# Kernel optimization log

Hardware: AMD Instinct MI355X
Metric: run time of the kernel (lower is better)

Reference implementation:

```python
import jax, jax.numpy as jnp
import numpy as np

H = 4096      # hidden_size
NH = 32       # num heads
HD = H // NH  # head_dim = 128
I = 11008     # intermediate_size
T = 1024      # prompt tokens
G = 128       # AWQ group size
EPS = 1e-6
ROPE_BASE = 10000.0


def _pack4(key, in_f, out_f):
    # pack 8 uint4 nibbles per int32, [in_f, out_f/8]
    nib = jax.random.randint(key, (in_f, out_f // 8, 8), 0, 16, dtype=jnp.int32)
    shifts = (jnp.arange(8, dtype=jnp.int32) * 4)
    return jnp.bitwise_or.reduce(nib << shifts, axis=-1).astype(jnp.int32)


def _dequant(qw, qz, sc):
    # qw:[in,out/8] int32, qz:[in/G,out/8] int32, sc:[in/G,out] float
    shifts = jnp.arange(8, dtype=jnp.int32) * 4
    w = ((qw[:, :, None] >> shifts) & 0xF).reshape(qw.shape[0], -1)   # [in,out]
    z = ((qz[:, :, None] >> shifts) & 0xF).reshape(qz.shape[0], -1)   # [groups,out]
    gidx = jnp.arange(qw.shape[0]) // G
    return (w.astype(sc.dtype) - z.astype(sc.dtype)[gidx]) * sc[gidx]


def _qlinear(x, qw, qz, sc):
    return x @ _dequant(qw, qz, sc)


def _rmsnorm(x, w):
    var = jnp.mean(x * x, axis=-1, keepdims=True)
    return x * jax.lax.rsqrt(var + EPS) * w


def _rope(x, positions):
    # x: [T, NH, HD], neox-style half rotation (vLLM rotary)
    inv = 1.0 / (ROPE_BASE ** (jnp.arange(0, HD, 2, dtype=jnp.float32) / HD))
    freqs = positions.astype(jnp.float32)[:, None] * inv[None, :]     # [T, HD/2]
    cos = jnp.cos(freqs)[:, None, :]
    sin = jnp.sin(freqs)[:, None, :]
    x1, x2 = jnp.split(x, 2, axis=-1)
    return jnp.concatenate([x1 * cos - x2 * sin, x2 * cos + x1 * sin], axis=-1)


def _attention(positions, q, k, v):
    # causal self-attention over the prompt (prefill writes k/v to cache then attends)
    q = _rope(q.reshape(T, NH, HD), positions)
    k = _rope(k.reshape(T, NH, HD), positions)
    v = v.reshape(T, NH, HD)
    scale = HD ** -0.5
    scores = jnp.einsum('qhd,khd->hqk', q, k) * scale
    mask = jnp.tril(jnp.ones((T, T), dtype=bool))
    scores = jnp.where(mask[None], scores, jnp.finfo(scores.dtype).min)
    probs = jax.nn.softmax(scores, axis=-1)
    out = jnp.einsum('hqk,khd->qhd', probs, v)
    return out.reshape(T, NH * HD)


def setup_inputs() -> dict:
    key = jax.random.key(0)
    ks = jax.random.split(key, 16)
    S = 0.002  # AWQ scale magnitude
    inp = {
        'positions': jnp.arange(T, dtype=jnp.int32),
        'hidden_states': jax.random.normal(ks[0], (T, H), dtype=jnp.float32),
        'ln1_w': jnp.ones((H,), dtype=jnp.float32),
        'ln2_w': jnp.ones((H,), dtype=jnp.float32),
        'qkv_qw': _pack4(ks[1], H, 3 * H),
        'qkv_qz': _pack4(ks[2], H // G, 3 * H),
        'qkv_sc': jax.random.uniform(ks[3], (H // G, 3 * H), dtype=jnp.float32) * S,
        'o_qw': _pack4(ks[4], H, H),
        'o_qz': _pack4(ks[5], H // G, H),
        'o_sc': jax.random.uniform(ks[6], (H // G, H), dtype=jnp.float32) * S,
        'gate_qw': _pack4(ks[7], H, I),
        'gate_qz': _pack4(ks[8], H // G, I),
        'gate_sc': jax.random.uniform(ks[9], (H // G, I), dtype=jnp.float32) * S,
        'up_qw': _pack4(ks[10], H, I),
        'up_qz': _pack4(ks[11], H // G, I),
        'up_sc': jax.random.uniform(ks[12], (H // G, I), dtype=jnp.float32) * S,
        'down_qw': _pack4(ks[13], I, H),
        'down_qz': _pack4(ks[14], I // G, H),
        'down_sc': jax.random.uniform(ks[15], (I // G, H), dtype=jnp.float32) * S,
    }
    return inp


def reference(positions, hidden_states, ln1_w, qkv_qw, qkv_qz, qkv_sc,
              o_qw, o_qz, o_sc, gate_qw, gate_qz, gate_sc,
              up_qw, up_qz, up_sc, down_qw, down_qz, down_sc, ln2_w):
    # --- self attention block ---
    residual = hidden_states
    x = _rmsnorm(hidden_states, ln1_w)
    qkv = _qlinear(x, qkv_qw, qkv_qz, qkv_sc)                # [T, 3H]
    q, k, v = jnp.split(qkv, 3, axis=-1)
    attn_out = _attention(positions, q, k, v)                # [T, H]
    x = _qlinear(attn_out, o_qw, o_qz, o_sc)
    hidden = residual + x
    # --- MLP block ---
    residual = hidden
    x = _rmsnorm(hidden, ln2_w)
    gate = jax.nn.silu(_qlinear(x, gate_qw, gate_qz, gate_sc))
    up = _qlinear(x, up_qw, up_qz, up_sc)
    x = _qlinear(gate * up, down_qw, down_qz, down_sc)
    return residual + x
```

## Files before the change

### kernel.cpp

```cpp
#include <hip/hip_runtime.h>
#include <cstdint>

typedef __attribute__((ext_vector_type(8))) short  bf16x8;
typedef __attribute__((ext_vector_type(4))) float  f32x4;
typedef __attribute__((ext_vector_type(4))) unsigned int uint4v;
typedef __attribute__((ext_vector_type(2))) unsigned int uint2v;

typedef const __attribute__((address_space(1))) void* gas_t;
typedef __attribute__((address_space(3))) void* las_t;

__device__ __forceinline__ float bf2f(unsigned short b) {
    union { unsigned int u; float f; } v; v.u = ((unsigned int)b) << 16; return v.f;
}
__device__ __forceinline__ unsigned short f2bf(float f) {
    union { float f; unsigned int u; } v; v.f = f;
    unsigned int r = v.u + 0x7FFFu + ((v.u >> 16) & 1u);
    return (unsigned short)(r >> 16);
}
__device__ __forceinline__ float u2f(unsigned int u) {
    union { unsigned int u; float f; } v; v.u = u; return v.f;
}

__device__ __forceinline__ void dequant_block(int bx, int by, int t,
    const int* __restrict__ qw, const int* __restrict__ qz,
    const float* __restrict__ sc, unsigned short* __restrict__ out,
    int NW, int K)
{
    const int wcb = bx << 5;
    const int kb  = by << 6;
    const int g   = by >> 1;
    const int N   = NW << 3;
    const int wc  = wcb + (t >> 3);
    const int k0  = kb + ((t & 7) << 3);

    unsigned int w[8];
#pragma unroll
    for (int j = 0; j < 8; j++) w[j] = (unsigned int)qw[(size_t)(k0 + j) * NW + wc];
    const unsigned int zw = (unsigned int)qz[(size_t)g * NW + wc];
    float scv[8];
#pragma unroll
    for (int j2 = 0; j2 < 8; j2++) scv[j2] = sc[(size_t)g * N + (wc << 3) + j2];

#pragma unroll
    for (int j2 = 0; j2 < 8; j2++) {
        const int sh = j2 << 2;
        const float s = scv[j2];
        const float moff = -(8388608.0f + (float)((zw >> sh) & 0xFu)) * s;
        unsigned int pk[4];
#pragma unroll
        for (int i = 0; i < 4; i++) {
            float f0 = fmaf(u2f(((w[2*i]   >> sh) & 0xFu) | 0x4B000000u), s, moff);
            float f1 = fmaf(u2f(((w[2*i+1] >> sh) & 0xFu) | 0x4B000000u), s, moff);
            asm("v_cvt_pk_bf16_f32 %0, %1, %2" : "=v"(pk[i]) : "v"(f0), "v"(f1));
        }
        uint4v ov = {pk[0], pk[1], pk[2], pk[3]};
        *(uint4v*)(out + (size_t)((wc << 3) + j2) * K + k0) = ov;
    }
}

__global__ __launch_bounds__(256)
void deq_rms_kernel(const int* __restrict__ qw, const int* __restrict__ qz,
                    const float* __restrict__ sc, unsigned short* __restrict__ wout,
                    int NW, int K, int deqBlocks,
                    const float* __restrict__ x, const float* __restrict__ lnw,
                    unsigned short* __restrict__ xout)
{
    __shared__ float red[4];
    const int tid = threadIdx.x;
    if (blockIdx.x < (unsigned)deqBlocks) {
        int xb = NW >> 5;
        dequant_block(blockIdx.x % xb, blockIdx.x / xb, tid, qw, qz, sc, wout, NW, K);
        return;
    }
    const int t = blockIdx.x - deqBlocks;
    const float4* xr = (const float4*)(x + (size_t)t * 4096);
    float4 v[4];
    float ss = 0.f;
#pragma unroll
    for (int j = 0; j < 4; j++) {
        v[j] = xr[(j << 8) + tid];
        ss += v[j].x*v[j].x + v[j].y*v[j].y + v[j].z*v[j].z + v[j].w*v[j].w;
    }
#pragma unroll
    for (int m = 1; m < 64; m <<= 1) ss += __shfl_xor(ss, m);
    if ((tid & 63) == 0) red[tid >> 6] = ss;
    __syncthreads();
    float tot = red[0] + red[1] + red[2] + red[3];
    float rs = rsqrtf(tot * (1.f / 4096.f) + 1e-6f);
    const float4* wr = (const float4*)lnw;
#pragma unroll
    for (int j = 0; j < 4; j++) {
        float4 wv = wr[(j << 8) + tid];
        float4 xv = v[j];
        unsigned int p0 = (unsigned int)f2bf(xv.x*rs*wv.x) | ((unsigned int)f2bf(xv.y*rs*wv.y) << 16);
        unsigned int p1 = (unsigned int)f2bf(xv.z*rs*wv.z) | ((unsigned int)f2bf(xv.w*rs*wv.w) << 16);
        uint2v pk = {p0, p1};
        *(uint2v*)(&xout[(size_t)t*4096 + (size_t)(((j << 8) + tid) << 2)]) = pk;
    }
}

__global__ __launch_bounds__(256)
void rmsnorm_kernel(const float* __restrict__ x, const float* __restrict__ wgt,
                    unsigned short* __restrict__ out)
{
    const int t = blockIdx.x, tid = threadIdx.x;
    const float4* xr = (const float4*)(x + (size_t)t * 4096);
    float4 v[4];
    float ss = 0.f;
#pragma unroll
    for (int j = 0; j < 4; j++) {
        v[j] = xr[(j << 8) + tid];
        ss += v[j].x*v[j].x + v[j].y*v[j].y + v[j].z*v[j].z + v[j].w*v[j].w;
    }
#pragma unroll
    for (int m = 1; m < 64; m <<= 1) ss += __shfl_xor(ss, m);
    __shared__ float red[4];
    if ((tid & 63) == 0) red[tid >> 6] = ss;
    __syncthreads();
    float tot = red[0] + red[1] + red[2] + red[3];
    float rs = rsqrtf(tot * (1.f / 4096.f) + 1e-6f);
    const float4* wr = (const float4*)wgt;
#pragma unroll
    for (int j = 0; j < 4; j++) {
        float4 wv = wr[(j << 8) + tid];
        float4 xv = v[j];
        unsigned int p0 = (unsigned int)f2bf(xv.x*rs*wv.x) | ((unsigned int)f2bf(xv.y*rs*wv.y) << 16);
        unsigned int p1 = (unsigned int)f2bf(xv.z*rs*wv.z) | ((unsigned int)f2bf(xv.w*rs*wv.w) << 16);
        uint2v pk = {p0, p1};
        *(uint2v*)(&out[(size_t)t*4096 + (size_t)(((j << 8) + tid) << 2)]) = pk;
    }
}

template<int MODE>
__global__ __launch_bounds__(256, 4)
void bt_gemm(const unsigned short* __restrict__ A,
             const unsigned short* __restrict__ Bt0,
             const unsigned short* __restrict__ Bt1,
             void* __restrict__ out0, void* __restrict__ out1,
             const float* __restrict__ res,
             int N, int K, int NB, int gemmBlocks, int ksplit,
             const int* dq1_qw, const int* dq1_qz, const float* dq1_sc,
             unsigned short* dq1_out, int dq1_NW, int dq1_K)
{
    const int flat = blockIdx.x;
    if (flat >= gemmBlocks) {
        if (blockIdx.z != 0) return;
        int db = flat - gemmBlocks;
        int xb = dq1_NW >> 5;
        dequant_block(db % xb, db / xb, threadIdx.x, dq1_qw, dq1_qz, dq1_sc, dq1_out, dq1_NW, dq1_K);
        return;
    }

    const int work = NB * (flat & 7) + (flat >> 3);
    const int n0 = (work >> 3) << 7;
    const int m0 = (work & 7) << 7;
    const int z  = blockIdx.z;

    const unsigned short* Bt = Bt0;
    void* outp = out0;
    if (MODE == 1 && z == 1) { Bt = Bt1; outp = out1; }
    const int k0base = (MODE == 2) ? z * ksplit : 0;
    const int nsteps = ((MODE == 2) ? ksplit : K) >> 6;

    __shared__ unsigned short As[128 * 64];
    __shared__ unsigned short Bs[128 * 64];

    const int tid  = threadIdx.x;
    const int lane = tid & 63;
    const int wid  = tid >> 6;
    const int wm   = wid >> 1, wn = wid & 1;

    f32x4 acc[4][4];
#pragma unroll
    for (int i = 0; i < 4; i++)
#pragma unroll
        for (int j = 0; j < 4; j++) { f32x4 zv = {0.f,0.f,0.f,0.f}; acc[i][j] = zv; }

    for (int t = 0; t < nsteps; t++) {
        const int k0 = k0base + (t << 6);
        __syncthreads();
#pragma unroll
        for (int i = 0; i < 4; i++) {
            int slot = (i << 8) + tid;
            int row = slot >> 3, s = slot & 7;
            __builtin_amdgcn_global_load_lds(
                (gas_t)(A + (size_t)(m0 + row) * K + k0 + ((s ^ (row & 7)) << 3)),
                (las_t)&As[slot << 3], 16, 0, 0);
        }
#pragma unroll
        for (int i = 0; i < 4; i++) {
            int slot = (i << 8) + tid;
            int row = slot >> 3, s = slot & 7;
            __builtin_amdgcn_global_load_lds(
                (gas_t)(Bt + (size_t)(n0 + row) * K + k0 + ((s ^ (row & 7)) << 3)),
                (las_t)&Bs[slot << 3], 16, 0, 0);
        }
        __syncthreads();
#pragma unroll
        for (int kk = 0; kk < 2; kk++) {
            const int srow = (kk << 2) + (lane >> 4);
            bf16x8 af[4], bfv[4];
#pragma unroll
            for (int mi = 0; mi < 4; mi++) {
                int r = (wm << 6) + (mi << 4) + (lane & 15);
                af[mi] = *(const bf16x8*)(&As[(r << 6) + ((srow ^ (r & 7)) << 3)]);
            }
#pragma unroll
            for (int ni = 0; ni < 4; ni++) {
                int r = (wn << 6) + (ni << 4) + (lane & 15);
                bfv[ni] = *(const bf16x8*)(&Bs[(r << 6) + ((srow ^ (r & 7)) << 3)]);
            }
#pragma unroll
            for (int mi = 0; mi < 4; mi++)
#pragma unroll
                for (int ni = 0; ni < 4; ni++)
                    acc[mi][ni] = __builtin_amdgcn_mfma_f32_16x16x32_bf16(af[mi], bfv[ni], acc[mi][ni], 0, 0, 0);
        }
    }

    const int rbase = m0 + (wm << 6) + ((lane >> 4) << 2);
    const int cbase = n0 + (wn << 6) + (lane & 15);
#pragma unroll
    for (int mi = 0; mi < 4; mi++) {
#pragma unroll
        for (int r = 0; r < 4; r++) {
            int row = rbase + (mi << 4) + r;
#pragma unroll
            for (int ni = 0; ni < 4; ni++) {
                int col = cbase + (ni << 4);
                float v = acc[mi][ni][r];
                if (MODE == 3) {
                    ((float*)out0)[(size_t)row * N + col] = v + res[(size_t)row * N + col];
                } else if (MODE == 2) {
                    ((unsigned short*)out0)[(size_t)z * ((size_t)1024 * N) + (size_t)row * N + col] = f2bf(v);
                } else {
                    ((unsigned short*)outp)[(size_t)row * N + col] = f2bf(v);
                }
            }
        }
    }
}

__global__ __launch_bounds__(256)
void reduce4_kernel(const float* __restrict__ base, const unsigned short* __restrict__ part,
                    float* __restrict__ out)
{
    const size_t i = (size_t)blockIdx.x * 256 + threadIdx.x;
    const size_t stride = (size_t)1024 * 4096;
    float s[8];
    float4 a0 = ((const float4*)base)[2*i], a1 = ((const float4*)base)[2*i+1];
    s[0]=a0.x; s[1]=a0.y; s[2]=a0.z; s[3]=a0.w; s[4]=a1.x; s[5]=a1.y; s[6]=a1.z; s[7]=a1.w;
#pragma unroll
    for (int p = 0; p < 4; p++) {
        uint4v v = *(const uint4v*)(part + p * stride + i * 8);
#pragma unroll
        for (int j = 0; j < 4; j++) {
            s[2*j]   += bf2f((unsigned short)(v[j] & 0xFFFF));
            s[2*j+1] += bf2f((unsigned short)(v[j] >> 16));
        }
    }
    float4 o0 = {s[0],s[1],s[2],s[3]}, o1 = {s[4],s[5],s[6],s[7]};
    ((float4*)out)[2*i] = o0; ((float4*)out)[2*i+1] = o1;
}

__global__ __launch_bounds__(256)
void rope_kernel(const int* __restrict__ positions, const unsigned short* __restrict__ qkv,
                 unsigned short* __restrict__ Qr, unsigned short* __restrict__ Kr,
                 unsigned short* __restrict__ Vtp)
{
    const int t = blockIdx.x, tid = threadIdx.x;
    const float p = (float)positions[t];
    const unsigned short* row = qkv + (size_t)t * 12288;
#pragma unroll 4
    for (int it = 0; it < 16; it++) {
        int task = (it << 8) + tid;
        int i   = task & 63;
        int hh  = (task >> 6) & 31;
        int isK = task >> 11;
        float fr = p * __expf(-(float)i * 0.14391156831f);
        float s, c;
        __sincosf(fr, &s, &c);
        const unsigned short* src = row + (isK << 12) + (hh << 7);
        float x1 = bf2f(src[i]);
        float x2 = bf2f(src[64 + i]);
        float o1 = x1 * c - x2 * s;
        float o2 = x2 * c + x1 * s;
        if (!isK) { o1 *= 0.08838834764831845f; o2 *= 0.08838834764831845f; }
        unsigned short* dst = (isK ? Kr : Qr) + ((size_t)hh * 1024 + t) * 128;
        dst[i]      = f2bf(o1);
        dst[64 + i] = f2bf(o2);
    }
#pragma unroll 4
    for (int it = 0; it < 16; it++) {
        int task = (it << 8) + tid;
        int d = task & 127, hh = task >> 7;
        Vtp[((size_t)hh * 128 + d) * 1024 + t] = row[8192 + task];
    }
}

__global__ __launch_bounds__(256, 2)
void attn_kernel(const unsigned short* __restrict__ Qr, const unsigned short* __restrict__ Kr,
                 const unsigned short* __restrict__ Vtp, unsigned short* __restrict__ attn_out,
                 int attnBlocks,
                 const int* __restrict__ dqw, const int* __restrict__ dqz,
                 const float* __restrict__ dsc, unsigned short* __restrict__ dwout,
                 int dNW, int dK)
{
    if (blockIdx.x >= (unsigned)attnBlocks) {
        int db = blockIdx.x - attnBlocks;
        int xb = dNW >> 5;
        dequant_block(db % xb, db / xb, threadIdx.x, dqw, dqz, dsc, dwout, dNW, dK);
        return;
    }
    __shared__ unsigned short Ks[64 * 128];
    __shared__ unsigned short Vs[128 * 64];
    __shared__ unsigned short Ps[4][16 * 64];
    const int tid = threadIdx.x, lane = tid & 63, w = tid >> 6;
    const int qt = blockIdx.x & 15, h = blockIdx.x >> 4;

    const unsigned short* Qh = Qr + ((size_t)h * 1024 + (size_t)qt * 64) * 128;

    bf16x8 qf[4];
#pragma unroll
    for (int kk = 0; kk < 4; kk++)
        qf[kk] = *(const bf16x8*)(Qh + (size_t)((w << 4) + (lane & 15)) * 128 + (kk << 5) + ((lane >> 4) << 3));

    f32x4 o[8];
#pragma unroll
    for (int i = 0; i < 8; i++) { f32x4 zf = {0.f,0.f,0.f,0.f}; o[i] = zf; }
    float Mr[4] = {-1e30f, -1e30f, -1e30f, -1e30f};
    float Lr[4] = {0.f, 0.f, 0.f, 0.f};
    const int qrow0 = (qt << 6) + (w << 4) + ((lane >> 4) << 2);

    for (int kt = 0; kt <= qt; kt++) {
        __syncthreads();
#pragma unroll
        for (int j = 0; j < 4; j++) {
            int slot = (j << 8) + tid;
            int rw = slot >> 4, s = slot & 15;
            int ssrc = (s & 8) | ((s ^ (rw & 7)) & 7);
            const uint4v* src = (const uint4v*)(Kr + ((size_t)h * 1024 + (size_t)kt * 64 + rw) * 128 + (ssrc << 3));
            *(uint4v*)(&Ks[(rw << 7) + (s << 3)]) = *src;
        }
#pragma unroll
        for (int j = 0; j < 4; j++) {
            int slot = (j << 8) + tid;
            int rw = slot >> 3, s = slot & 7;
            const uint4v* src = (const uint4v*)(Vtp + ((size_t)h * 128 + rw) * 1024 + (kt << 6) + ((s ^ (rw & 7)) << 3));
            *(uint4v*)(&Vs[(rw << 6) + (s << 3)]) = *src;
        }
        __syncthreads();

        f32x4 sc4[4];
#pragma unroll
        for (int ni = 0; ni < 4; ni++) { f32x4 zf = {0.f,0.f,0.f,0.f}; sc4[ni] = zf; }
#pragma unroll
        for (int kk = 0; kk < 4; kk++) {
#pragma unroll
            for (int ni = 0; ni < 4; ni++) {
                int r = (ni << 4) + (lane & 15);
                int s = (kk << 2) + (lane >> 4);
                int sp = (s & 8) | ((s ^ (r & 7)) & 7);
                bf16x8 kf = *(const bf16x8*)(&Ks[(r << 7) + (sp << 3)]);
                sc4[ni] = __builtin_amdgcn_mfma_f32_16x16x32_bf16(qf[kk], kf, sc4[ni], 0, 0, 0);
            }
        }

#pragma unroll
        for (int r = 0; r < 4; r++) {
            int qg = qrow0 + r;
            float mx = -1e30f;
#pragma unroll
            for (int ni = 0; ni < 4; ni++) {
                int kg_ = (kt << 6) + (ni << 4) + (lane & 15);
                float v = sc4[ni][r];
                if (kt == qt && kg_ > qg) { v = -1e30f; sc4[ni][r] = v; }
                mx = fmaxf(mx, v);
            }
#pragma unroll
            for (int m_ = 1; m_ < 16; m_ <<= 1) mx = fmaxf(mx, __shfl_xor(mx, m_));
            float mnew  = fmaxf(Mr[r], mx);
            float alpha = __expf(Mr[r] - mnew);
            Mr[r] = mnew;
            float rs = 0.f;
#pragma unroll
            for (int ni = 0; ni < 4; ni++) {
                float pv = __expf(sc4[ni][r] - mnew);
                sc4[ni][r] = pv;
                rs += pv;
            }
#pragma unroll
            for (int m_ = 1; m_ < 16; m_ <<= 1) rs += __shfl_xor(rs, m_);
            Lr[r] = Lr[r] * alpha + rs;
#pragma unroll
            for (int nd = 0; nd < 8; nd++) o[nd][r] *= alpha;
        }

#pragma unroll
        for (int r = 0; r < 4; r++) {
            int qr = ((lane >> 4) << 2) + r;
#pragma unroll
            for (int ni = 0; ni < 4; ni++) {
                int col = (ni << 4) + (lane & 15);
                int phys = (col >> 3) ^ (qr & 7);
                Ps[w][(qr << 6) + (phys << 3) + (col & 7)] = f2bf(sc4[ni][r]);
            }
        }
#pragma unroll
        for (int kk2 = 0; kk2 < 2; kk2++) {
            int rowp = lane & 15;
            int sl = (kk2 << 2) + (lane >> 4);
            bf16x8 pa = *(const bf16x8*)(&Ps[w][(rowp << 6) + ((sl ^ (rowp & 7)) << 3)]);
#pragma unroll
            for (int nd = 0; nd < 8; nd++) {
                int rv = (nd << 4) + (lane & 15);
                bf16x8 vb = *(const bf16x8*)(&Vs[(rv << 6) + ((sl ^ (rv & 7)) << 3)]);
                o[nd] = __builtin_amdgcn_mfma_f32_16x16x32_bf16(pa, vb, o[nd], 0, 0, 0);
            }
        }
    }

#pragma unroll
    for (int r = 0; r < 4; r++) {
        float inv = 1.0f / Lr[r];
        int trow = qrow0 + r;
#pragma unroll
        for (int nd = 0; nd < 8; nd++) {
            int col = (h << 7) + (nd << 4) + (lane & 15);
            attn_out[(size_t)trow * 4096 + col] = f2bf(o[nd][r] * inv);
        }
    }
}

__global__ __launch_bounds__(256)
void silu_deq_kernel(const unsigned short* __restrict__ gate, unsigned short* __restrict__ up,
                     int siluBlocks,
                     const int* __restrict__ qw, const int* __restrict__ qz,
                     const float* __restrict__ sc, unsigned short* __restrict__ wout,
                     int NW, int K)
{
    if (blockIdx.x >= (unsigned)siluBlocks) {
        int db = blockIdx.x - siluBlocks;
        int xb = NW >> 5;
        dequant_block(db % xb, db / xb, threadIdx.x, qw, qz, sc, wout, NW, K);
        return;
    }
    size_t idx = ((size_t)blockIdx.x * 256 + threadIdx.x) * 8;
    uint4v g = *(const uint4v*)(gate + idx);
    uint4v u = *(const uint4v*)(up + idx);
    unsigned int outp[4];
#pragma unroll
    for (int j = 0; j < 4; j++) {
        unsigned int gw = g[j], uw = u[j];
        float g0 = bf2f((unsigned short)(gw & 0xFFFF)), g1 = bf2f((unsigned short)(gw >> 16));
        float u0 = bf2f((unsigned short)(uw & 0xFFFF)), u1 = bf2f((unsigned short)(uw >> 16));
        float s0 = g0 / (1.f + __expf(-g0)) * u0;
        float s1 = g1 / (1.f + __expf(-g1)) * u1;
        outp[j] = (unsigned int)f2bf(s0) | ((unsigned int)f2bf(s1) << 16);
    }
    uint4v ov = {outp[0], outp[1], outp[2], outp[3]};
    *(uint4v*)(up + idx) = ov;
}

extern "C" void kernel_launch(void* const* d_in, const int* in_sizes, int n_in,
                              void* d_out, int out_size, void* d_ws, size_t ws_size,
                              hipStream_t stream)
{
    const int*   positions = (const int*)  d_in[0];
    const float* hidden    = (const float*)d_in[1];
    const float* ln1       = (const float*)d_in[2];
    const float* ln2       = (const float*)d_in[3];
    const int*   qkv_qw    = (const int*)  d_in[4];
    const int*   qkv_qz    = (const int*)  d_in[5];
    const float* qkv_sc    = (const float*)d_in[6];
    const int*   o_qw      = (const int*)  d_in[7];
    const int*   o_qz      = (const int*)  d_in[8];
    const float* o_sc      = (const float*)d_in[9];
    const int*   gate_qw   = (const int*)  d_in[10];
    const int*   gate_qz   = (const int*)  d_in[11];
    const float* gate_sc   = (const float*)d_in[12];
    const int*   up_qw     = (const int*)  d_in[13];
    const int*   up_qz     = (const int*)  d_in[14];
    const float* up_sc     = (const float*)d_in[15];
    const int*   down_qw   = (const int*)  d_in[16];
    const int*   down_qz   = (const int*)  d_in[17];
    const float* down_sc   = (const float*)d_in[18];

    char* ws = (char*)d_ws;
    const size_t MB = 1 << 20;
    unsigned short* W_qkv = (unsigned short*)(ws + 0);
    unsigned short* Qrp   = (unsigned short*)(ws + 0);
    unsigned short* Krp   = (unsigned short*)(ws + 8 * MB);
    unsigned short* Vtp   = (unsigned short*)(ws + 16 * MB);
    unsigned short* W_gate= (unsigned short*)(ws + 0);
    unsigned short* W_down= (unsigned short*)(ws + 0);
    unsigned short* attnb = (unsigned short*)(ws + 86 * MB);
    unsigned short* W_o   = (unsigned short*)(ws + 96 * MB);
    unsigned short* gateb = (unsigned short*)(ws + 96 * MB);
    unsigned short* part  = (unsigned short*)(ws + 96 * MB);
    unsigned short* W_up  = (unsigned short*)(ws + 128 * MB);
    unsigned short* xln   = (unsigned short*)(ws + 214 * MB);
    unsigned short* qkvb  = (unsigned short*)(ws + 222 * MB);
    unsigned short* upb   = (unsigned short*)(ws + 222 * MB);
    float*          hid   = (float*)d_out;

    deq_rms_kernel<<<3072 + 1024, 256, 0, stream>>>(
        qkv_qw, qkv_qz, qkv_sc, W_qkv, 1536, 4096, 3072,
        hidden, ln1, xln);
    bt_gemm<0><<<768 + 1024, 256, 0, stream>>>(
        xln, W_qkv, nullptr, (void*)qkvb, nullptr, nullptr,
        12288, 4096, 96, 768, 0,
        o_qw, o_qz, o_sc, W_o, 512, 4096);
    rope_kernel<<<1024, 256, 0, stream>>>(positions, qkvb, Qrp, Krp, Vtp);
    attn_kernel<<<512 + 2752, 256, 0, stream>>>(
        Qrp, Krp, Vtp, attnb, 512,
        up_qw, up_qz, up_sc, W_up, 1376, 4096);
    bt_gemm<3><<<256 + 2752, 256, 0, stream>>>(
        attnb, W_o, nullptr, (void*)hid, nullptr, hidden,
        4096, 4096, 32, 256, 0,
        gate_qw, gate_qz, gate_sc, W_gate, 1376, 4096);
    rmsnorm_kernel<<<1024, 256, 0, stream>>>(hid, ln2, xln);
    bt_gemm<1><<<dim3(688, 1, 2), 256, 0, stream>>>(
        xln, W_gate, W_up, (void*)gateb, (void*)upb, nullptr,
        11008, 4096, 86, 688, 0,
        nullptr, nullptr, nullptr, nullptr, 32, 64);
    silu_deq_kernel<<<5504 + 2752, 256, 0, stream>>>(
        gateb, upb, 5504, down_qw, down_qz, down_sc, W_down, 512, 11008);
    bt_gemm<2><<<dim3(256, 1, 4), 256, 0, stream>>>(
        upb, W_down, nullptr, (void*)part, nullptr, nullptr,
        4096, 11008, 32, 256, 2752,
        nullptr, nullptr, nullptr, nullptr, 32, 64);
    reduce4_kernel<<<2048, 256, 0, stream>>>(hid, part, (float*)d_out);
}
```

Baseline: 680.4 us.

## Fuse SiLU-multiply into gate GEMM epilogue and drop separate silu kernel

The combined gate/up GEMM launch is split into two launches: first the up projection, then the gate projection, whose epilogue reads the up output, applies SiLU(gate)*up and writes the product in place. The down-weight dequant blocks now ride on the gate GEMM launch instead of the removed standalone silu kernel. Workspace buffers are reshuffled so W_down and the split-K partials do not collide with live data. Launch bounds are raised to 5 blocks per CU, which may constrain registers. This saves the gate buffer round-trip and one elementwise pass, but serializes the two GEMMs.

```diff
diff --git a/kernel.cpp b/kernel.cpp
--- a/kernel.cpp
+++ b/kernel.cpp
@@ -132,7 +132,7 @@
 }
 
 template<int MODE>
-__global__ __launch_bounds__(256, 4)
+__global__ __launch_bounds__(256, 5)
 void bt_gemm(const unsigned short* __restrict__ A,
              const unsigned short* __restrict__ Bt0,
              const unsigned short* __restrict__ Bt1,
@@ -157,8 +157,6 @@
     const int z  = blockIdx.z;
 
     const unsigned short* Bt = Bt0;
-    void* outp = out0;
-    if (MODE == 1 && z == 1) { Bt = Bt1; outp = out1; }
     const int k0base = (MODE == 2) ? z * ksplit : 0;
     const int nsteps = ((MODE == 2) ? ksplit : K) >> 6;
 
@@ -233,8 +231,12 @@
                     ((float*)out0)[(size_t)row * N + col] = v + res[(size_t)row * N + col];
                 } else if (MODE == 2) {
                     ((unsigned short*)out0)[(size_t)z * ((size_t)1024 * N) + (size_t)row * N + col] = f2bf(v);
+                } else if (MODE == 4) {
+                    float u = bf2f(((const unsigned short*)out1)[(size_t)row * N + col]);
+                    float sv = v / (1.f + __expf(-v)) * u;
+                    ((unsigned short*)out0)[(size_t)row * N + col] = f2bf(sv);
                 } else {
-                    ((unsigned short*)outp)[(size_t)row * N + col] = f2bf(v);
+                    ((unsigned short*)out0)[(size_t)row * N + col] = f2bf(v);
                 }
             }
         }
@@ -432,36 +434,6 @@
     }
 }
 
-__global__ __launch_bounds__(256)
-void silu_deq_kernel(const unsigned short* __restrict__ gate, unsigned short* __restrict__ up,
-                     int siluBlocks,
-                     const int* __restrict__ qw, const int* __restrict__ qz,
-                     const float* __restrict__ sc, unsigned short* __restrict__ wout,
-                     int NW, int K)
-{
-    if (blockIdx.x >= (unsigned)siluBlocks) {
-        int db = blockIdx.x - siluBlocks;
-        int xb = NW >> 5;
-        dequant_block(db % xb, db / xb, threadIdx.x, qw, qz, sc, wout, NW, K);
-        return;
-    }
-    size_t idx = ((size_t)blockIdx.x * 256 + threadIdx.x) * 8;
-    uint4v g = *(const uint4v*)(gate + idx);
-    uint4v u = *(const uint4v*)(up + idx);
-    unsigned int outp[4];
-#pragma unroll
-    for (int j = 0; j < 4; j++) {
-        unsigned int gw = g[j], uw = u[j];
-        float g0 = bf2f((unsigned short)(gw & 0xFFFF)), g1 = bf2f((unsigned short)(gw >> 16));
-        float u0 = bf2f((unsigned short)(uw & 0xFFFF)), u1 = bf2f((unsigned short)(uw >> 16));
-        float s0 = g0 / (1.f + __expf(-g0)) * u0;
-        float s1 = g1 / (1.f + __expf(-g1)) * u1;
-        outp[j] = (unsigned int)f2bf(s0) | ((unsigned int)f2bf(s1) << 16);
-    }
-    uint4v ov = {outp[0], outp[1], outp[2], outp[3]};
-    *(uint4v*)(up + idx) = ov;
-}
-
 extern "C" void kernel_launch(void* const* d_in, const int* in_sizes, int n_in,
                               void* d_out, int out_size, void* d_ws, size_t ws_size,
                               hipStream_t stream)
@@ -493,11 +465,10 @@
     unsigned short* Krp   = (unsigned short*)(ws + 8 * MB);
     unsigned short* Vtp   = (unsigned short*)(ws + 16 * MB);
     unsigned short* W_gate= (unsigned short*)(ws + 0);
-    unsigned short* W_down= (unsigned short*)(ws + 0);
+    unsigned short* part  = (unsigned short*)(ws + 0);
     unsigned short* attnb = (unsigned short*)(ws + 86 * MB);
     unsigned short* W_o   = (unsigned short*)(ws + 96 * MB);
-    unsigned short* gateb = (unsigned short*)(ws + 96 * MB);
-    unsigned short* part  = (unsigned short*)(ws + 96 * MB);
+    unsigned short* W_down= (unsigned short*)(ws + 96 * MB);
     unsigned short* W_up  = (unsigned short*)(ws + 128 * MB);
     unsigned short* xln   = (unsigned short*)(ws + 214 * MB);
     unsigned short* qkvb  = (unsigned short*)(ws + 222 * MB);
@@ -520,12 +491,14 @@
         4096, 4096, 32, 256, 0,
         gate_qw, gate_qz, gate_sc, W_gate, 1376, 4096);
     rmsnorm_kernel<<<1024, 256, 0, stream>>>(hid, ln2, xln);
-    bt_gemm<1><<<dim3(688, 1, 2), 256, 0, stream>>>(
-        xln, W_gate, W_up, (void*)gateb, (void*)upb, nullptr,
+    bt_gemm<0><<<688, 256, 0, stream>>>(
+        xln, W_up, nullptr, (void*)upb, nullptr, nullptr,
         11008, 4096, 86, 688, 0,
         nullptr, nullptr, nullptr, nullptr, 32, 64);
-    silu_deq_kernel<<<5504 + 2752, 256, 0, stream>>>(
-        gateb, upb, 5504, down_qw, down_qz, down_sc, W_down, 512, 11008);
+    bt_gemm<4><<<688 + 2752, 256, 0, stream>>>(
+        xln, W_gate, nullptr, (void*)upb, (void*)upb, nullptr,
+        11008, 4096, 86, 688, 0,
+        down_qw, down_qz, down_sc, W_down, 512, 11008);
     bt_gemm<2><<<dim3(256, 1, 4), 256, 0, stream>>>(
         upb, W_down, nullptr, (void*)part, nullptr, nullptr,
         4096, 11008, 32, 256, 2752,
```

Result: slower. 1.289 ms (+89.4%).

## Split-K the o_proj GEMM in two and fuse reduction with residual and RMSNorm

Applied to the files above, without the earlier changes.

The o_proj GEMM (256 output tiles, too few to fill the GPU) is now split along K into two halves via a z-dimension of 2, each writing bf16 partials. A new kernel sums both partials with the residual, writes the hidden state, and applies the second RMSNorm in the same pass, replacing the separate rmsnorm kernel and the fused residual-add epilogue. This raises parallelism for the small GEMM. The cost is extra partial-buffer traffic and bf16 rounding of the partial sums. The piggybacked dequant blocks return early for z != 0, so only the GEMM part is doubled.

```diff
diff --git a/kernel.cpp b/kernel.cpp
--- a/kernel.cpp
+++ b/kernel.cpp
@@ -99,45 +99,12 @@
     }
 }
 
-__global__ __launch_bounds__(256)
-void rmsnorm_kernel(const float* __restrict__ x, const float* __restrict__ wgt,
-                    unsigned short* __restrict__ out)
-{
-    const int t = blockIdx.x, tid = threadIdx.x;
-    const float4* xr = (const float4*)(x + (size_t)t * 4096);
-    float4 v[4];
-    float ss = 0.f;
-#pragma unroll
-    for (int j = 0; j < 4; j++) {
-        v[j] = xr[(j << 8) + tid];
-        ss += v[j].x*v[j].x + v[j].y*v[j].y + v[j].z*v[j].z + v[j].w*v[j].w;
-    }
-#pragma unroll
-    for (int m = 1; m < 64; m <<= 1) ss += __shfl_xor(ss, m);
-    __shared__ float red[4];
-    if ((tid & 63) == 0) red[tid >> 6] = ss;
-    __syncthreads();
-    float tot = red[0] + red[1] + red[2] + red[3];
-    float rs = rsqrtf(tot * (1.f / 4096.f) + 1e-6f);
-    const float4* wr = (const float4*)wgt;
-#pragma unroll
-    for (int j = 0; j < 4; j++) {
-        float4 wv = wr[(j << 8) + tid];
-        float4 xv = v[j];
-        unsigned int p0 = (unsigned int)f2bf(xv.x*rs*wv.x) | ((unsigned int)f2bf(xv.y*rs*wv.y) << 16);
-        unsigned int p1 = (unsigned int)f2bf(xv.z*rs*wv.z) | ((unsigned int)f2bf(xv.w*rs*wv.w) << 16);
-        uint2v pk = {p0, p1};
-        *(uint2v*)(&out[(size_t)t*4096 + (size_t)(((j << 8) + tid) << 2)]) = pk;
-    }
-}
-
 template<int MODE>
 __global__ __launch_bounds__(256, 4)
 void bt_gemm(const unsigned short* __restrict__ A,
              const unsigned short* __restrict__ Bt0,
              const unsigned short* __restrict__ Bt1,
              void* __restrict__ out0, void* __restrict__ out1,
-             const float* __restrict__ res,
              int N, int K, int NB, int gemmBlocks, int ksplit,
              const int* dq1_qw, const int* dq1_qz, const float* dq1_sc,
              unsigned short* dq1_out, int dq1_NW, int dq1_K)
@@ -229,15 +196,57 @@
             for (int ni = 0; ni < 4; ni++) {
                 int col = cbase + (ni << 4);
                 float v = acc[mi][ni][r];
-                if (MODE == 3) {
-                    ((float*)out0)[(size_t)row * N + col] = v + res[(size_t)row * N + col];
-                } else if (MODE == 2) {
+                if (MODE == 2) {
                     ((unsigned short*)out0)[(size_t)z * ((size_t)1024 * N) + (size_t)row * N + col] = f2bf(v);
                 } else {
                     ((unsigned short*)outp)[(size_t)row * N + col] = f2bf(v);
                 }
             }
         }
+    }
+}
+
+__global__ __launch_bounds__(256)
+void reduce2o_rms(const float* __restrict__ base, const unsigned short* __restrict__ part,
+                  const float* __restrict__ lnw,
+                  float* __restrict__ hid, unsigned short* __restrict__ xout)
+{
+    __shared__ float red[4];
+    const int t = blockIdx.x, tid = threadIdx.x;
+    const size_t stride = (size_t)1024 * 4096;
+    const float4* xr = (const float4*)(base + (size_t)t * 4096);
+    const uint2v* p0 = (const uint2v*)(part + (size_t)t * 4096);
+    const uint2v* p1 = (const uint2v*)(part + stride + (size_t)t * 4096);
+    float4* hw = (float4*)(hid + (size_t)t * 4096);
+    float4 v[4];
+    float ss = 0.f;
+#pragma unroll
+    for (int i = 0; i < 4; i++) {
+        float4 a = xr[(i << 8) + tid];
+        uint2v b0 = p0[(i << 8) + tid];
+        uint2v b1 = p1[(i << 8) + tid];
+        a.x += bf2f((unsigned short)(b0[0] & 0xFFFF)) + bf2f((unsigned short)(b1[0] & 0xFFFF));
+        a.y += bf2f((unsigned short)(b0[0] >> 16))    + bf2f((unsigned short)(b1[0] >> 16));
+        a.z += bf2f((unsigned short)(b0[1] & 0xFFFF)) + bf2f((unsigned short)(b1[1] & 0xFFFF));
+        a.w += bf2f((unsigned short)(b0[1] >> 16))    + bf2f((unsigned short)(b1[1] >> 16));
+        v[i] = a;
+        ss += a.x*a.x + a.y*a.y + a.z*a.z + a.w*a.w;
+        hw[(i << 8) + tid] = a;
+    }
+#pragma unroll
+    for (int m = 1; m < 64; m <<= 1) ss += __shfl_xor(ss, m);
+    if ((tid & 63) == 0) red[tid >> 6] = ss;
+    __syncthreads();
+    float tot = red[0] + red[1] + red[2] + red[3];
+    float rs = rsqrtf(tot * (1.f / 4096.f) + 1e-6f);
+    const float4* wr = (const float4*)lnw;
+#pragma unroll
+    for (int i = 0; i < 4; i++) {
+        float4 wv = wr[(i << 8) + tid];
+        unsigned int q0 = (unsigned int)f2bf(v[i].x*rs*wv.x) | ((unsigned int)f2bf(v[i].y*rs*wv.y) << 16);
+        unsigned int q1 = (unsigned int)f2bf(v[i].z*rs*wv.z) | ((unsigned int)f2bf(v[i].w*rs*wv.w) << 16);
+        uint2v pk = {q0, q1};
+        *(uint2v*)(&xout[(size_t)t*4096 + (size_t)(((i << 8) + tid) << 2)]) = pk;
     }
 }
 
@@ -501,6 +510,7 @@
     unsigned short* W_up  = (unsigned short*)(ws + 128 * MB);
     unsigned short* xln   = (unsigned short*)(ws + 214 * MB);
     unsigned short* qkvb  = (unsigned short*)(ws + 222 * MB);
+    unsigned short* part_o= (unsigned short*)(ws + 222 * MB);
     unsigned short* upb   = (unsigned short*)(ws + 222 * MB);
     float*          hid   = (float*)d_out;
 
@@ -508,26 +518,26 @@
         qkv_qw, qkv_qz, qkv_sc, W_qkv, 1536, 4096, 3072,
         hidden, ln1, xln);
     bt_gemm<0><<<768 + 1024, 256, 0, stream>>>(
-        xln, W_qkv, nullptr, (void*)qkvb, nullptr, nullptr,
+        xln, W_qkv, nullptr, (void*)qkvb, nullptr,
         12288, 4096, 96, 768, 0,
         o_qw, o_qz, o_sc, W_o, 512, 4096);
     rope_kernel<<<1024, 256, 0, stream>>>(positions, qkvb, Qrp, Krp, Vtp);
     attn_kernel<<<512 + 2752, 256, 0, stream>>>(
         Qrp, Krp, Vtp, attnb, 512,
         up_qw, up_qz, up_sc, W_up, 1376, 4096);
-    bt_gemm<3><<<256 + 2752, 256, 0, stream>>>(
-        attnb, W_o, nullptr, (void*)hid, nullptr, hidden,
-        4096, 4096, 32, 256, 0,
+    bt_gemm<2><<<dim3(256 + 2752, 1, 2), 256, 0, stream>>>(
+        attnb, W_o, nullptr, (void*)part_o, nullptr,
+        4096, 4096, 32, 256, 2048,
         gate_qw, gate_qz, gate_sc, W_gate, 1376, 4096);
-    rmsnorm_kernel<<<1024, 256, 0, stream>>>(hid, ln2, xln);
+    reduce2o_rms<<<1024, 256, 0, stream>>>(hidden, part_o, ln2, hid, xln);
     bt_gemm<1><<<dim3(688, 1, 2), 256, 0, stream>>>(
-        xln, W_gate, W_up, (void*)gateb, (void*)upb, nullptr,
+        xln, W_gate, W_up, (void*)gateb, (void*)upb,
         11008, 4096, 86, 688, 0,
         nullptr, nullptr, nullptr, nullptr, 32, 64);
     silu_deq_kernel<<<5504 + 2752, 256, 0, stream>>>(
         gateb, upb, 5504, down_qw, down_qz, down_sc, W_down, 512, 11008);
     bt_gemm<2><<<dim3(256, 1, 4), 256, 0, stream>>>(
-        upb, W_down, nullptr, (void*)part, nullptr, nullptr,
+        upb, W_down, nullptr, (void*)part, nullptr,
         4096, 11008, 32, 256, 2752,
         nullptr, nullptr, nullptr, nullptr, 32, 64);
     reduce4_kernel<<<2048, 256, 0, stream>>>(hid, part, (float*)d_out);
```

Result: no change. 670.9 us (median of 2 runs) (-1.4%).
